# Performance work log

Hardware: AMD Instinct MI355X
Metric: run time of the kernel (lower is better)

## Reference

```python
import jax, jax.numpy as jnp
import numpy as np


def _ln(x):
    m = jnp.mean(x, axis=-1, keepdims=True)
    v = jnp.var(x, axis=-1, keepdims=True)
    return (x - m) * jax.lax.rsqrt(v + 1e-5)


def _forward(ql, cl, plm, ada_g_w, ada_g_b, ada_b_w, wq, bq, wk, wv, z_ln_g, z_ln_b, wz, wg, wo, sg_w, sg_b, ada2_g_w, ada2_g_b, ada2_b_w, ff1, ff2, ff3, sg2_w, sg2_b, n_queries, n_keys):
    B, N, C = ql.shape
    NB, _, D = wq.shape
    H = wz.shape[-1]
    DH = D // H
    # AF3-style 32x128 blocked local attention bias (additive mask), as in source
    centers = jnp.arange(N // n_queries + 1, dtype=jnp.float32) * n_queries + (n_queries / 2 - 0.5)
    pos = jnp.arange(N, dtype=jnp.float32)
    row = jnp.abs(pos[:, None] - centers[None, :]) < n_queries / 2   # [N, n_centers]
    col = jnp.abs(pos[:, None] - centers[None, :]) < n_keys / 2     # [N, n_centers]
    BIG = jnp.float32(1e10)
    blm = jnp.sum((row[:, None, :] & col[None, :, :]).astype(jnp.float32), axis=-1) * BIG - BIG  # [N, N], 0 or -1e10
    s_ln = _ln(cl)  # conditioning signal, shared LN across blocks
    a = ql
    for i in range(NB):  # DiffusionTransformer (AF3 Alg 23)
        # AttentionPairBias with AdaLN conditioning (Alg 24/26)
        x = jax.nn.sigmoid(s_ln @ ada_g_w[i] + ada_g_b[i]) * _ln(a) + s_ln @ ada_b_w[i]
        q = (x @ wq[i] + bq[i]).reshape(B, N, H, DH)
        k = (x @ wk[i]).reshape(B, N, H, DH)
        v = (x @ wv[i]).reshape(B, N, H, DH)
        zb = jnp.einsum('bqkc,ch->bhqk', _ln(plm) * z_ln_g[i] + z_ln_b[i], wz[i])  # pair bias
        logits = jnp.einsum('bqhd,bkhd->bhqk', q, k) * (1.0 / np.sqrt(DH)) + zb + blm[None, None]
        p = jax.nn.softmax(logits, axis=-1)
        o = jnp.einsum('bhqk,bkhd->bqhd', p, v)
        g = jax.nn.sigmoid(x @ wg[i]).reshape(B, N, H, DH)
        attn = (g * o).reshape(B, N, D) @ wo[i]
        b_out = jax.nn.sigmoid(s_ln @ sg_w[i] + sg_b[i]) * attn  # adaLN-zero style output gate
        # ConditionedTransitionBlock (Alg 25, SwiGLU)
        y = jax.nn.sigmoid(s_ln @ ada2_g_w[i] + ada2_g_b[i]) * _ln(a) + s_ln @ ada2_b_w[i]
        ff = jax.nn.silu(y @ ff1[i]) * (y @ ff2[i])
        t = jax.nn.sigmoid(s_ln @ sg2_w[i] + sg2_b[i]) * (ff @ ff3[i])
        a = b_out + t
    return a


def setup_inputs() -> dict:
    key = jax.random.key(0)
    B, N, C, CZ = 1, 3072, 128, 16
    H, DH, NB, CT = 4, 32, 3, 256  # CT = n_transition * C
    D = H * DH
    ks = jax.random.split(key, 32)
    it = iter(range(32))
    def r(shape, s=0.02):
        return jax.random.normal(ks[next(it)], shape, dtype=jnp.float32) * s
    inp = {
        'ql': jax.random.normal(ks[next(it)], (B, N, C), jnp.float32),
        'cl': jax.random.normal(ks[next(it)], (B, N, C), jnp.float32),
        'plm': jax.random.normal(ks[next(it)], (B, N, N, CZ), jnp.float32),
        'ada_g_w': r((NB, C, C)), 'ada_g_b': jnp.zeros((NB, C), jnp.float32), 'ada_b_w': r((NB, C, C)),
        'wq': r((NB, C, D)), 'bq': jnp.zeros((NB, D), jnp.float32), 'wk': r((NB, C, D)), 'wv': r((NB, C, D)),
        'z_ln_g': jnp.ones((NB, CZ), jnp.float32), 'z_ln_b': jnp.zeros((NB, CZ), jnp.float32), 'wz': r((NB, CZ, H)),
        'wg': r((NB, C, D)), 'wo': r((NB, D, C)),
        'sg_w': r((NB, C, C)), 'sg_b': jnp.full((NB, C), -2.0, jnp.float32),
        'ada2_g_w': r((NB, C, C)), 'ada2_g_b': jnp.zeros((NB, C), jnp.float32), 'ada2_b_w': r((NB, C, C)),
        'ff1': r((NB, C, CT)), 'ff2': r((NB, C, CT)), 'ff3': r((NB, CT, C)),
        'sg2_w': r((NB, C, C)), 'sg2_b': jnp.full((NB, C), -2.0, jnp.float32),
        'n_queries': 32, 'n_keys': 128,
    }
    return inp


def reference(ql, cl, plm, ada_g_w, ada_g_b, ada_b_w, wq, bq, wk, wv, z_ln_g, z_ln_b, wz, wg, wo, sg_w, sg_b, ada2_g_w, ada2_g_b, ada2_b_w, ff1, ff2, ff3, sg2_w, sg2_b, n_queries, n_keys):
    return _forward(ql, cl, plm, ada_g_w, ada_g_b, ada_b_w, wq, bq, wk, wv, z_ln_g, z_ln_b, wz, wg, wo, sg_w, sg_b, ada2_g_w, ada2_g_b, ada2_b_w, ff1, ff2, ff3, sg2_w, sg2_b, n_queries, n_keys)
```

## Files before the change

### kernel.cpp

```cpp
#include <hip/hip_runtime.h>
#include <cmath>

#define NTOK 3072
#define NBLK 3
#define PSS 133

__device__ __forceinline__ float sig(float v) { return 1.0f / (1.0f + expf(-v)); }

struct Params {
    const float *ql, *cl, *plm;
    const float *ada_g_w, *ada_g_b, *ada_b_w;
    const float *wq, *bq, *wk, *wv;
    const float *z_ln_g, *z_ln_b, *wz;
    const float *wg, *wo, *sg_w, *sg_b;
    const float *ada2_g_w, *ada2_g_b, *ada2_b_w;
    const float *ff1, *ff2, *ff3, *sg2_w, *sg2_b;
    float *anew, *attn, *qkvg, *ffb, *zb, *G;
    float *out;
};

__device__ __forceinline__ float4 ln_row32(float4 v)
{
    float s = v.x + v.y + v.z + v.w;
#pragma unroll
    for (int m = 1; m < 32; m <<= 1) s += __shfl_xor(s, m);
    float mean = s * (1.0f / 128.0f);
    float d0 = v.x - mean, d1 = v.y - mean, d2 = v.z - mean, d3 = v.w - mean;
    float var = d0 * d0 + d1 * d1 + d2 * d2 + d3 * d3;
#pragma unroll
    for (int m = 1; m < 32; m <<= 1) var += __shfl_xor(var, m);
    float rs = 1.0f / sqrtf(var * (1.0f / 128.0f) + 1e-5f);
    return make_float4(d0 * rs, d1 * rs, d2 * rs, d3 * rs);
}

__global__ __launch_bounds__(256) void k0_cond(Params P)
{
    int tid = threadIdx.x, bid = blockIdx.x;
    const size_t NC = (size_t)NTOK * 128;
    if (bid < 1728) {
        __shared__ __align__(16) float smA[32 * 132];
        int x8 = bid & 7, rest = bid >> 3;
        int tl = rest % 12, unit = rest / 12;
        int kind = unit % 6, i = unit / 6;
        int row0 = (x8 * 12 + tl) * 32;
#pragma unroll
        for (int it = 0; it < 4; it++) {
            int fo = (tid + it * 256) * 4, r = fo >> 7, c = fo & 127;
            *(float4*)&smA[r * 132 + c] = *(const float4*)&P.cl[(size_t)(row0 + r) * 128 + c];
        }
        __syncthreads();
        int hw = tid >> 5, cq = (tid & 31) * 4;
#pragma unroll
        for (int rr = 0; rr < 4; rr++) {
            int r = hw * 4 + rr;
            float4 n = ln_row32(*(float4*)&smA[r * 132 + cq]);
            *(float4*)&smA[r * 132 + cq] = n;
        }
        __syncthreads();
        const float* W; const float* bias = nullptr; bool dosig = false;
        switch (kind) {
            case 0:  W = P.ada_g_w  + (size_t)i * 16384; bias = P.ada_g_b  + i * 128; dosig = true; break;
            case 1:  W = P.ada_b_w  + (size_t)i * 16384; break;
            case 2:  W = P.ada2_g_w + (size_t)i * 16384; bias = P.ada2_g_b + i * 128; dosig = true; break;
            case 3:  W = P.ada2_b_w + (size_t)i * 16384; break;
            case 4:  W = P.sg_w     + (size_t)i * 16384; bias = P.sg_b     + i * 128; dosig = true; break;
            default: W = P.sg2_w    + (size_t)i * 16384; bias = P.sg2_b    + i * 128; dosig = true; break;
        }
        W += cq;
        float acc[4][4] = {};
#pragma unroll 8
        for (int k = 0; k < 128; k++) {
            float4 w4 = *(const float4*)(W + (size_t)k * 128);
#pragma unroll
            for (int rr = 0; rr < 4; rr++) {
                float a = smA[(hw * 4 + rr) * 132 + k];
                acc[rr][0] = fmaf(a, w4.x, acc[rr][0]);
                acc[rr][1] = fmaf(a, w4.y, acc[rr][1]);
                acc[rr][2] = fmaf(a, w4.z, acc[rr][2]);
                acc[rr][3] = fmaf(a, w4.w, acc[rr][3]);
            }
        }
        float4 b4 = bias ? *(const float4*)&bias[cq] : make_float4(0, 0, 0, 0);
        float* dst = P.G + (size_t)(kind * NBLK + i) * NC;
#pragma unroll
        for (int rr = 0; rr < 4; rr++) {
            float4 o = make_float4(acc[rr][0] + b4.x, acc[rr][1] + b4.y,
                                   acc[rr][2] + b4.z, acc[rr][3] + b4.w);
            if (dosig) { o.x = sig(o.x); o.y = sig(o.y); o.z = sig(o.z); o.w = sig(o.w); }
            *(float4*)&dst[(size_t)(row0 + hw * 4 + rr) * 128 + cq] = o;
        }
    } else {
        __shared__ __align__(16) float wzg[204];
        int b2 = bid - 1728;
        int x8 = b2 & 7, rest = b2 >> 3;
        int jl = rest >> 2, kkc = rest & 3;
        int j = x8 * 12 + jl;
        if (tid < 192) {
            int i3 = tid >> 6, rem = tid & 63, c = rem >> 2, h = rem & 3;
            wzg[(i3 * 16 + c) * 4 + h] = P.z_ln_g[i3 * 16 + c] * P.wz[(i3 * 16 + c) * 4 + h];
        }
        if (tid < 12) {
            int i3 = tid >> 2, h = tid & 3;
            float s = 0.0f;
            for (int c = 0; c < 16; c++) s += P.z_ln_b[i3 * 16 + c] * P.wz[(i3 * 16 + c) * 4 + h];
            wzg[192 + tid] = s;
        }
        __syncthreads();
        int kstart = max(0, j * 32 - 48);
        int W = min(NTOK, j * 32 + 80) - kstart;
#pragma unroll
        for (int it = 0; it < 4; it++) {
            int idx = tid + it * 256;
            int qi = idx >> 5, kk = kkc * 32 + (idx & 31);
            if (kk >= W) continue;
            int q = j * 32 + qi;
            const float* src = P.plm + ((size_t)q * NTOK + (size_t)(kstart + kk)) * 16;
            float xv[16];
            *(float4*)(xv + 0)  = *(const float4*)(src + 0);
            *(float4*)(xv + 4)  = *(const float4*)(src + 4);
            *(float4*)(xv + 8)  = *(const float4*)(src + 8);
            *(float4*)(xv + 12) = *(const float4*)(src + 12);
            float s = 0.0f;
#pragma unroll
            for (int c = 0; c < 16; c++) s += xv[c];
            float mean = s * (1.0f / 16.0f);
            float var = 0.0f;
#pragma unroll
            for (int c = 0; c < 16; c++) { float d = xv[c] - mean; var += d * d; }
            float rs = 1.0f / sqrtf(var * (1.0f / 16.0f) + 1e-5f);
#pragma unroll
            for (int c = 0; c < 16; c++) xv[c] = (xv[c] - mean) * rs;
#pragma unroll
            for (int i3 = 0; i3 < NBLK; i3++) {
#pragma unroll
                for (int h = 0; h < 4; h++) {
                    float o = wzg[192 + i3 * 4 + h];
#pragma unroll
                    for (int c = 0; c < 16; c++) o = fmaf(xv[c], wzg[(i3 * 16 + c) * 4 + h], o);
                    P.zb[((size_t)(i3 * 4 + h) * NTOK + q) * 128 + kk] = o;
                }
            }
        }
    }
}

__global__ __launch_bounds__(256) void k1_pre(Params P, int i)
{
    __shared__ __align__(16) float smX[16 * 132];
    const size_t NC = (size_t)NTOK * 128;
    int tid = threadIdx.x, bid = blockIdx.x;
    int x8 = bid & 7, rest = bid >> 3;
    int tl = rest % 24, u = rest / 24;
    int row0 = (x8 * 24 + tl) * 16;
    int sg = tid >> 5, cq = (tid & 31) * 4;
    const float* aprev = (i == 0) ? P.ql : P.anew;
    const float* Gg = P.G + (size_t)(((u < 4 ? 0 : 2) * NBLK) + i) * NC;
    const float* Gb = P.G + (size_t)(((u < 4 ? 1 : 3) * NBLK) + i) * NC;
#pragma unroll
    for (int rr = 0; rr < 2; rr++) {
        int r = row0 + sg * 2 + rr;
        float4 a4 = *(const float4*)&aprev[(size_t)r * 128 + cq];
        float4 ln4 = ln_row32(a4);
        float4 g4 = *(const float4*)&Gg[(size_t)r * 128 + cq];
        float4 b4 = *(const float4*)&Gb[(size_t)r * 128 + cq];
        float4 x4;
        x4.x = fmaf(g4.x, ln4.x, b4.x);
        x4.y = fmaf(g4.y, ln4.y, b4.y);
        x4.z = fmaf(g4.z, ln4.z, b4.z);
        x4.w = fmaf(g4.w, ln4.w, b4.w);
        *(float4*)&smX[(sg * 2 + rr) * 132 + cq] = x4;
    }
    __syncthreads();
    if (u < 4) {
        const float* W = (u == 0 ? P.wq : u == 1 ? P.wk : u == 2 ? P.wv : P.wg)
                         + (size_t)i * 16384 + cq;
        float acc[2][4] = {};
#pragma unroll 8
        for (int k = 0; k < 128; k++) {
            float4 w4 = *(const float4*)(W + (size_t)k * 128);
#pragma unroll
            for (int rr = 0; rr < 2; rr++) {
                float a = smX[(sg * 2 + rr) * 132 + k];
                acc[rr][0] = fmaf(a, w4.x, acc[rr][0]);
                acc[rr][1] = fmaf(a, w4.y, acc[rr][1]);
                acc[rr][2] = fmaf(a, w4.z, acc[rr][2]);
                acc[rr][3] = fmaf(a, w4.w, acc[rr][3]);
            }
        }
        float4 b4 = (u == 0) ? *(const float4*)&P.bq[(size_t)i * 128 + cq]
                             : make_float4(0, 0, 0, 0);
#pragma unroll
        for (int rr = 0; rr < 2; rr++) {
            int r = row0 + sg * 2 + rr;
            *(float4*)&P.qkvg[(size_t)r * 512 + u * 128 + cq] =
                make_float4(acc[rr][0] + b4.x, acc[rr][1] + b4.y,
                            acc[rr][2] + b4.z, acc[rr][3] + b4.w);
        }
    } else {
        int ch = (u - 4) * 128;
        const float* W1 = P.ff1 + (size_t)i * 32768 + ch + cq;
        const float* W2 = P.ff2 + (size_t)i * 32768 + ch + cq;
        float a1[2][4] = {}, a2[2][4] = {};
#pragma unroll 8
        for (int k = 0; k < 128; k++) {
            float4 w14 = *(const float4*)(W1 + (size_t)k * 256);
            float4 w24 = *(const float4*)(W2 + (size_t)k * 256);
#pragma unroll
            for (int rr = 0; rr < 2; rr++) {
                float a = smX[(sg * 2 + rr) * 132 + k];
                a1[rr][0] = fmaf(a, w14.x, a1[rr][0]);
                a1[rr][1] = fmaf(a, w14.y, a1[rr][1]);
                a1[rr][2] = fmaf(a, w14.z, a1[rr][2]);
                a1[rr][3] = fmaf(a, w14.w, a1[rr][3]);
                a2[rr][0] = fmaf(a, w24.x, a2[rr][0]);
                a2[rr][1] = fmaf(a, w24.y, a2[rr][1]);
                a2[rr][2] = fmaf(a, w24.z, a2[rr][2]);
                a2[rr][3] = fmaf(a, w24.w, a2[rr][3]);
            }
        }
#pragma unroll
        for (int rr = 0; rr < 2; rr++) {
            int r = row0 + sg * 2 + rr;
            float4 o;
            o.x = a1[rr][0] * sig(a1[rr][0]) * a2[rr][0];
            o.y = a1[rr][1] * sig(a1[rr][1]) * a2[rr][1];
            o.z = a1[rr][2] * sig(a1[rr][2]) * a2[rr][2];
            o.w = a1[rr][3] * sig(a1[rr][3]) * a2[rr][3];
            *(float4*)&P.ffb[(size_t)r * 256 + ch + cq] = o;
        }
    }
}

__global__ __launch_bounds__(256) void k2_attn(Params P, int i)
{
    __shared__ __align__(16) float ks[128 * 36];
    __shared__ __align__(16) float vs[128 * 36];
    __shared__ float ps[16 * PSS];
    int tid = threadIdx.x, bid = blockIdx.x;
    int x8 = bid & 7, g = bid >> 3;
    int jl = g >> 3, rem = g & 7;
    int h = rem >> 1, qh = rem & 1;
    int jglob = x8 * 12 + jl;
    int q0 = jglob * 32 + qh * 16;
    int kstart = max(0, jglob * 32 - 48);
    int W = min(NTOK, jglob * 32 + 80) - kstart;
    for (int idx = tid; idx < W * 8; idx += 256) {
        int kk = idx >> 3, d = (idx & 7) * 4;
        const float* base = &P.qkvg[(size_t)(kstart + kk) * 512 + 128 + h * 32 + d];
        float4 tK = *(const float4*)base;
        float4 tV = *(const float4*)(base + 128);
        *(float4*)&ks[kk * 36 + d] = tK;
        *(float4*)&vs[kk * 36 + d] = tV;
    }
    const float* zbase = &P.zb[((size_t)(i * 4 + h) * NTOK + q0) * 128];
#pragma unroll
    for (int it = 0; it < 2; it++) {
        int idx = tid + it * 256;
        int r = idx >> 5, c4 = (idx & 31) * 4;
        float4 z4 = *(const float4*)&zbase[(size_t)r * 128 + c4];
        ps[r * PSS + c4]     = z4.x;
        ps[r * PSS + c4 + 1] = z4.y;
        ps[r * PSS + c4 + 2] = z4.z;
        ps[r * PSS + c4 + 3] = z4.w;
    }
    int qi = tid & 15, kg = tid >> 4;
    float qreg[32];
    {
        const float* qp = &P.qkvg[(size_t)(q0 + qi) * 512 + h * 32];
#pragma unroll
        for (int d4 = 0; d4 < 8; d4++) {
            float4 tq = *(const float4*)(qp + d4 * 4);
            qreg[d4 * 4] = tq.x; qreg[d4 * 4 + 1] = tq.y;
            qreg[d4 * 4 + 2] = tq.z; qreg[d4 * 4 + 3] = tq.w;
        }
    }
    __syncthreads();
    const float scale = 0.17677669529663687f;
#pragma unroll
    for (int t2 = 0; t2 < 8; t2++) {
        int kk = kg + t2 * 16;
        if (kk < W) {
            float acc = 0.0f;
#pragma unroll
            for (int d4 = 0; d4 < 8; d4++) {
                float4 kv = *(const float4*)&ks[kk * 36 + d4 * 4];
                acc = fmaf(qreg[d4 * 4 + 0], kv.x, acc);
                acc = fmaf(qreg[d4 * 4 + 1], kv.y, acc);
                acc = fmaf(qreg[d4 * 4 + 2], kv.z, acc);
                acc = fmaf(qreg[d4 * 4 + 3], kv.w, acc);
            }
            ps[qi * PSS + kk] = fmaf(acc, scale, ps[qi * PSS + kk]);
        }
    }
    __syncthreads();
    {
        int row = tid >> 4, sub = tid & 15;
        float m = -3.0e38f;
        for (int kk = sub; kk < W; kk += 16) m = fmaxf(m, ps[row * PSS + kk]);
#pragma unroll
        for (int s2 = 1; s2 < 16; s2 <<= 1) m = fmaxf(m, __shfl_xor(m, s2));
        float ssum = 0.0f;
        for (int kk = sub; kk < W; kk += 16) {
            float e = expf(ps[row * PSS + kk] - m);
            ps[row * PSS + kk] = e; ssum += e;
        }
#pragma unroll
        for (int s2 = 1; s2 < 16; s2 <<= 1) ssum += __shfl_xor(ssum, s2);
        float rinv = 1.0f / ssum;
        for (int kk = sub; kk < W; kk += 16) ps[row * PSS + kk] *= rinv;
    }
    __syncthreads();
    {
        int dg = tid >> 4, d0 = dg * 2;
        float o0 = 0.0f, o1 = 0.0f, o0b = 0.0f, o1b = 0.0f;
        for (int kk = 0; kk + 1 < W; kk += 2) {
            float p0 = ps[qi * PSS + kk], p1 = ps[qi * PSS + kk + 1];
            float2 va = *(const float2*)&vs[kk * 36 + d0];
            float2 vb = *(const float2*)&vs[(kk + 1) * 36 + d0];
            o0  = fmaf(p0, va.x, o0);  o1  = fmaf(p0, va.y, o1);
            o0b = fmaf(p1, vb.x, o0b); o1b = fmaf(p1, vb.y, o1b);
        }
        if (W & 1) {
            float p0 = ps[qi * PSS + W - 1];
            float2 va = *(const float2*)&vs[(W - 1) * 36 + d0];
            o0 = fmaf(p0, va.x, o0); o1 = fmaf(p0, va.y, o1);
        }
        o0 += o0b; o1 += o1b;
        float2 g2 = *(const float2*)&P.qkvg[(size_t)(q0 + qi) * 512 + 384 + h * 32 + d0];
        *(float2*)&P.attn[(size_t)(q0 + qi) * 128 + h * 32 + d0] =
            make_float2(o0 * sig(g2.x), o1 * sig(g2.y));
    }
}

__global__ __launch_bounds__(256) void k3_post(Params P, int i)
{
    __shared__ __align__(16) float smB[16 * 132];
    __shared__ __align__(16) float smC[16 * 260];
    const size_t NC = (size_t)NTOK * 128;
    int tid = threadIdx.x, bid = blockIdx.x;
    int x8 = bid & 7, rest = bid >> 3;
    int tl = rest >> 2, cc = rest & 3;
    int row0 = x8 * 384 + tl * 16;
    int cbase = cc * 32;
#pragma unroll
    for (int it = 0; it < 2; it++) {
        int fo = (tid + it * 256) * 4, r = fo >> 7, c = fo & 127;
        *(float4*)&smB[r * 132 + c] = *(const float4*)&P.attn[(size_t)(row0 + r) * 128 + c];
    }
#pragma unroll
    for (int it = 0; it < 4; it++) {
        int fo = (tid + it * 256) * 4, r = fo >> 8, c = fo & 255;
        *(float4*)&smC[r * 260 + c] = *(const float4*)&P.ffb[(size_t)(row0 + r) * 256 + c];
    }
    __syncthreads();
    int r = tid >> 4, cl2 = (tid & 15) * 2;
    int c = cbase + cl2;
    const float* wo_p = P.wo  + (size_t)i * 16384 + c;
    const float* f3_p = P.ff3 + (size_t)i * 32768 + c;
    float aO0 = 0, aO1 = 0, aT0 = 0, aT1 = 0;
#pragma unroll 8
    for (int k = 0; k < 128; k++) {
        float2 w2 = *(const float2*)(wo_p + (size_t)k * 128);
        float a = smB[r * 132 + k];
        aO0 = fmaf(a, w2.x, aO0);
        aO1 = fmaf(a, w2.y, aO1);
    }
#pragma unroll 8
    for (int k = 0; k < 256; k++) {
        float2 w2 = *(const float2*)(f3_p + (size_t)k * 128);
        float a = smC[r * 260 + k];
        aT0 = fmaf(a, w2.x, aT0);
        aT1 = fmaf(a, w2.y, aT1);
    }
    int row = row0 + r;
    float2 sgv  = *(const float2*)&P.G[(size_t)(4 * NBLK + i) * NC + (size_t)row * 128 + c];
    float2 sg2v = *(const float2*)&P.G[(size_t)(5 * NBLK + i) * NC + (size_t)row * 128 + c];
    float2 o;
    o.x = sgv.x * aO0 + sg2v.x * aT0;
    o.y = sgv.y * aO1 + sg2v.y * aT1;
    float* dst = (i == NBLK - 1) ? P.out : P.anew;
    *(float2*)&dst[(size_t)row * 128 + c] = o;
}

extern "C" void kernel_launch(void* const* d_in, const int* in_sizes, int n_in,
                              void* d_out, int out_size, void* d_ws, size_t ws_size,
                              hipStream_t stream)
{
    Params P;
    P.ql       = (const float*)d_in[0];
    P.cl       = (const float*)d_in[1];
    P.plm      = (const float*)d_in[2];
    P.ada_g_w  = (const float*)d_in[3];
    P.ada_g_b  = (const float*)d_in[4];
    P.ada_b_w  = (const float*)d_in[5];
    P.wq       = (const float*)d_in[6];
    P.bq       = (const float*)d_in[7];
    P.wk       = (const float*)d_in[8];
    P.wv       = (const float*)d_in[9];
    P.z_ln_g   = (const float*)d_in[10];
    P.z_ln_b   = (const float*)d_in[11];
    P.wz       = (const float*)d_in[12];
    P.wg       = (const float*)d_in[13];
    P.wo       = (const float*)d_in[14];
    P.sg_w     = (const float*)d_in[15];
    P.sg_b     = (const float*)d_in[16];
    P.ada2_g_w = (const float*)d_in[17];
    P.ada2_g_b = (const float*)d_in[18];
    P.ada2_b_w = (const float*)d_in[19];
    P.ff1      = (const float*)d_in[20];
    P.ff2      = (const float*)d_in[21];
    P.ff3      = (const float*)d_in[22];
    P.sg2_w    = (const float*)d_in[23];
    P.sg2_b    = (const float*)d_in[24];

    float* ws = (float*)d_ws;
    const size_t NC = (size_t)NTOK * 128;
    P.anew = ws;
    P.attn = ws + NC;
    P.qkvg = ws + 2 * NC;
    P.ffb  = ws + 6 * NC;
    P.zb   = ws + 8 * NC;
    P.G    = ws + 20 * NC;
    P.out  = (float*)d_out;

    k0_cond<<<2112, 256, 0, stream>>>(P);
    for (int i = 0; i < NBLK; i++) {
        k1_pre<<<1152, 256, 0, stream>>>(P, i);
        k2_attn<<<768, 256, 0, stream>>>(P, i);
        k3_post<<<768, 256, 0, stream>>>(P, i);
    }
}
```

Baseline: 325.1 us.

## Fuse output projection into attention and defer residual sum to next pre-kernel

The wo projection is folded into the attention kernel, with each head writing a partial output to a per-head buffer. The ff3 projection now runs in extra blocks of the same launch, and the gated sum that forms the new activation is deferred into the next block's pre-kernel, plus a small final combine kernel. This drops one launch per block and the attn round trip through memory. The pre-kernel also processes 32 rows per block instead of 16 to reuse weights more. In exchange there is extra traffic for four head-partial buffers and more register pressure in the pre-kernel.

```diff
diff --git a/kernel.cpp b/kernel.cpp
--- a/kernel.cpp
+++ b/kernel.cpp
@@ -15,7 +15,7 @@
     const float *wg, *wo, *sg_w, *sg_b;
     const float *ada2_g_w, *ada2_g_b, *ada2_b_w;
     const float *ff1, *ff2, *ff3, *sg2_w, *sg2_b;
-    float *anew, *attn, *qkvg, *ffb, *zb, *G;
+    float *qkvg, *ffb, *zb, *G, *bout4, *tpart;
     float *out;
 };
 
@@ -144,22 +144,37 @@
     }
 }
 
-__global__ __launch_bounds__(256) void k1_pre(Params P, int i)
-{
-    __shared__ __align__(16) float smX[16 * 132];
+__global__ __launch_bounds__(256) void kA_pre(Params P, int i)
+{
+    __shared__ __align__(16) float smX[32 * 132];
     const size_t NC = (size_t)NTOK * 128;
     int tid = threadIdx.x, bid = blockIdx.x;
     int x8 = bid & 7, rest = bid >> 3;
-    int tl = rest % 24, u = rest / 24;
-    int row0 = (x8 * 24 + tl) * 16;
-    int sg = tid >> 5, cq = (tid & 31) * 4;
-    const float* aprev = (i == 0) ? P.ql : P.anew;
+    int tl = rest % 12, u = rest / 12;
+    int row0 = (x8 * 12 + tl) * 32;
+    int hw = tid >> 5, cq = (tid & 31) * 4;
     const float* Gg = P.G + (size_t)(((u < 4 ? 0 : 2) * NBLK) + i) * NC;
     const float* Gb = P.G + (size_t)(((u < 4 ? 1 : 3) * NBLK) + i) * NC;
-#pragma unroll
-    for (int rr = 0; rr < 2; rr++) {
-        int r = row0 + sg * 2 + rr;
-        float4 a4 = *(const float4*)&aprev[(size_t)r * 128 + cq];
+    const float* G4p = P.G + (size_t)(4 * NBLK + (i - 1)) * NC;
+#pragma unroll
+    for (int rr = 0; rr < 4; rr++) {
+        int r = row0 + hw * 4 + rr;
+        float4 a4;
+        if (i == 0) {
+            a4 = *(const float4*)&P.ql[(size_t)r * 128 + cq];
+        } else {
+            size_t off = (size_t)r * 128 + cq;
+            float4 p0 = *(const float4*)&P.bout4[off];
+            float4 p1 = *(const float4*)&P.bout4[NC + off];
+            float4 p2 = *(const float4*)&P.bout4[2 * NC + off];
+            float4 p3 = *(const float4*)&P.bout4[3 * NC + off];
+            float4 tp = *(const float4*)&P.tpart[off];
+            float4 gs = *(const float4*)&G4p[off];
+            a4.x = fmaf(gs.x, p0.x + p1.x + p2.x + p3.x, tp.x);
+            a4.y = fmaf(gs.y, p0.y + p1.y + p2.y + p3.y, tp.y);
+            a4.z = fmaf(gs.z, p0.z + p1.z + p2.z + p3.z, tp.z);
+            a4.w = fmaf(gs.w, p0.w + p1.w + p2.w + p3.w, tp.w);
+        }
         float4 ln4 = ln_row32(a4);
         float4 g4 = *(const float4*)&Gg[(size_t)r * 128 + cq];
         float4 b4 = *(const float4*)&Gb[(size_t)r * 128 + cq];
@@ -168,19 +183,19 @@
         x4.y = fmaf(g4.y, ln4.y, b4.y);
         x4.z = fmaf(g4.z, ln4.z, b4.z);
         x4.w = fmaf(g4.w, ln4.w, b4.w);
-        *(float4*)&smX[(sg * 2 + rr) * 132 + cq] = x4;
+        *(float4*)&smX[(hw * 4 + rr) * 132 + cq] = x4;
     }
     __syncthreads();
     if (u < 4) {
         const float* W = (u == 0 ? P.wq : u == 1 ? P.wk : u == 2 ? P.wv : P.wg)
                          + (size_t)i * 16384 + cq;
-        float acc[2][4] = {};
+        float acc[4][4] = {};
 #pragma unroll 8
         for (int k = 0; k < 128; k++) {
             float4 w4 = *(const float4*)(W + (size_t)k * 128);
 #pragma unroll
-            for (int rr = 0; rr < 2; rr++) {
-                float a = smX[(sg * 2 + rr) * 132 + k];
+            for (int rr = 0; rr < 4; rr++) {
+                float a = smX[(hw * 4 + rr) * 132 + k];
                 acc[rr][0] = fmaf(a, w4.x, acc[rr][0]);
                 acc[rr][1] = fmaf(a, w4.y, acc[rr][1]);
                 acc[rr][2] = fmaf(a, w4.z, acc[rr][2]);
@@ -190,8 +205,8 @@
         float4 b4 = (u == 0) ? *(const float4*)&P.bq[(size_t)i * 128 + cq]
                              : make_float4(0, 0, 0, 0);
 #pragma unroll
-        for (int rr = 0; rr < 2; rr++) {
-            int r = row0 + sg * 2 + rr;
+        for (int rr = 0; rr < 4; rr++) {
+            int r = row0 + hw * 4 + rr;
             *(float4*)&P.qkvg[(size_t)r * 512 + u * 128 + cq] =
                 make_float4(acc[rr][0] + b4.x, acc[rr][1] + b4.y,
                             acc[rr][2] + b4.z, acc[rr][3] + b4.w);
@@ -200,14 +215,14 @@
         int ch = (u - 4) * 128;
         const float* W1 = P.ff1 + (size_t)i * 32768 + ch + cq;
         const float* W2 = P.ff2 + (size_t)i * 32768 + ch + cq;
-        float a1[2][4] = {}, a2[2][4] = {};
-#pragma unroll 8
+        float a1[4][4] = {}, a2[4][4] = {};
+#pragma unroll 4
         for (int k = 0; k < 128; k++) {
             float4 w14 = *(const float4*)(W1 + (size_t)k * 256);
             float4 w24 = *(const float4*)(W2 + (size_t)k * 256);
 #pragma unroll
-            for (int rr = 0; rr < 2; rr++) {
-                float a = smX[(sg * 2 + rr) * 132 + k];
+            for (int rr = 0; rr < 4; rr++) {
+                float a = smX[(hw * 4 + rr) * 132 + k];
                 a1[rr][0] = fmaf(a, w14.x, a1[rr][0]);
                 a1[rr][1] = fmaf(a, w14.y, a1[rr][1]);
                 a1[rr][2] = fmaf(a, w14.z, a1[rr][2]);
@@ -219,8 +234,8 @@
             }
         }
 #pragma unroll
-        for (int rr = 0; rr < 2; rr++) {
-            int r = row0 + sg * 2 + rr;
+        for (int rr = 0; rr < 4; rr++) {
+            int r = row0 + hw * 4 + rr;
             float4 o;
             o.x = a1[rr][0] * sig(a1[rr][0]) * a2[rr][0];
             o.y = a1[rr][1] * sig(a1[rr][1]) * a2[rr][1];
@@ -231,155 +246,178 @@
     }
 }
 
-__global__ __launch_bounds__(256) void k2_attn(Params P, int i)
-{
-    __shared__ __align__(16) float ks[128 * 36];
-    __shared__ __align__(16) float vs[128 * 36];
-    __shared__ float ps[16 * PSS];
-    int tid = threadIdx.x, bid = blockIdx.x;
-    int x8 = bid & 7, g = bid >> 3;
-    int jl = g >> 3, rem = g & 7;
-    int h = rem >> 1, qh = rem & 1;
-    int jglob = x8 * 12 + jl;
-    int q0 = jglob * 32 + qh * 16;
-    int kstart = max(0, jglob * 32 - 48);
-    int W = min(NTOK, jglob * 32 + 80) - kstart;
-    for (int idx = tid; idx < W * 8; idx += 256) {
-        int kk = idx >> 3, d = (idx & 7) * 4;
-        const float* base = &P.qkvg[(size_t)(kstart + kk) * 512 + 128 + h * 32 + d];
-        float4 tK = *(const float4*)base;
-        float4 tV = *(const float4*)(base + 128);
-        *(float4*)&ks[kk * 36 + d] = tK;
-        *(float4*)&vs[kk * 36 + d] = tV;
-    }
-    const float* zbase = &P.zb[((size_t)(i * 4 + h) * NTOK + q0) * 128];
-#pragma unroll
-    for (int it = 0; it < 2; it++) {
-        int idx = tid + it * 256;
-        int r = idx >> 5, c4 = (idx & 31) * 4;
-        float4 z4 = *(const float4*)&zbase[(size_t)r * 128 + c4];
-        ps[r * PSS + c4]     = z4.x;
-        ps[r * PSS + c4 + 1] = z4.y;
-        ps[r * PSS + c4 + 2] = z4.z;
-        ps[r * PSS + c4 + 3] = z4.w;
-    }
-    int qi = tid & 15, kg = tid >> 4;
-    float qreg[32];
-    {
-        const float* qp = &P.qkvg[(size_t)(q0 + qi) * 512 + h * 32];
-#pragma unroll
-        for (int d4 = 0; d4 < 8; d4++) {
-            float4 tq = *(const float4*)(qp + d4 * 4);
-            qreg[d4 * 4] = tq.x; qreg[d4 * 4 + 1] = tq.y;
-            qreg[d4 * 4 + 2] = tq.z; qreg[d4 * 4 + 3] = tq.w;
-        }
-    }
-    __syncthreads();
-    const float scale = 0.17677669529663687f;
-#pragma unroll
-    for (int t2 = 0; t2 < 8; t2++) {
-        int kk = kg + t2 * 16;
-        if (kk < W) {
-            float acc = 0.0f;
-#pragma unroll
-            for (int d4 = 0; d4 < 8; d4++) {
-                float4 kv = *(const float4*)&ks[kk * 36 + d4 * 4];
-                acc = fmaf(qreg[d4 * 4 + 0], kv.x, acc);
-                acc = fmaf(qreg[d4 * 4 + 1], kv.y, acc);
-                acc = fmaf(qreg[d4 * 4 + 2], kv.z, acc);
-                acc = fmaf(qreg[d4 * 4 + 3], kv.w, acc);
-            }
-            ps[qi * PSS + kk] = fmaf(acc, scale, ps[qi * PSS + kk]);
-        }
-    }
-    __syncthreads();
-    {
-        int row = tid >> 4, sub = tid & 15;
-        float m = -3.0e38f;
-        for (int kk = sub; kk < W; kk += 16) m = fmaxf(m, ps[row * PSS + kk]);
-#pragma unroll
-        for (int s2 = 1; s2 < 16; s2 <<= 1) m = fmaxf(m, __shfl_xor(m, s2));
-        float ssum = 0.0f;
-        for (int kk = sub; kk < W; kk += 16) {
-            float e = expf(ps[row * PSS + kk] - m);
-            ps[row * PSS + kk] = e; ssum += e;
-        }
-#pragma unroll
-        for (int s2 = 1; s2 < 16; s2 <<= 1) ssum += __shfl_xor(ssum, s2);
-        float rinv = 1.0f / ssum;
-        for (int kk = sub; kk < W; kk += 16) ps[row * PSS + kk] *= rinv;
-    }
-    __syncthreads();
-    {
-        int dg = tid >> 4, d0 = dg * 2;
-        float o0 = 0.0f, o1 = 0.0f, o0b = 0.0f, o1b = 0.0f;
-        for (int kk = 0; kk + 1 < W; kk += 2) {
-            float p0 = ps[qi * PSS + kk], p1 = ps[qi * PSS + kk + 1];
-            float2 va = *(const float2*)&vs[kk * 36 + d0];
-            float2 vb = *(const float2*)&vs[(kk + 1) * 36 + d0];
-            o0  = fmaf(p0, va.x, o0);  o1  = fmaf(p0, va.y, o1);
-            o0b = fmaf(p1, vb.x, o0b); o1b = fmaf(p1, vb.y, o1b);
-        }
-        if (W & 1) {
-            float p0 = ps[qi * PSS + W - 1];
-            float2 va = *(const float2*)&vs[(W - 1) * 36 + d0];
-            o0 = fmaf(p0, va.x, o0); o1 = fmaf(p0, va.y, o1);
-        }
-        o0 += o0b; o1 += o1b;
-        float2 g2 = *(const float2*)&P.qkvg[(size_t)(q0 + qi) * 512 + 384 + h * 32 + d0];
-        *(float2*)&P.attn[(size_t)(q0 + qi) * 128 + h * 32 + d0] =
-            make_float2(o0 * sig(g2.x), o1 * sig(g2.y));
-    }
-}
-
-__global__ __launch_bounds__(256) void k3_post(Params P, int i)
-{
-    __shared__ __align__(16) float smB[16 * 132];
-    __shared__ __align__(16) float smC[16 * 260];
+__global__ __launch_bounds__(256) void kB_attn(Params P, int i)
+{
+    __shared__ __align__(16) float sm[11344];
     const size_t NC = (size_t)NTOK * 128;
     int tid = threadIdx.x, bid = blockIdx.x;
-    int x8 = bid & 7, rest = bid >> 3;
-    int tl = rest >> 2, cc = rest & 3;
-    int row0 = x8 * 384 + tl * 16;
-    int cbase = cc * 32;
-#pragma unroll
-    for (int it = 0; it < 2; it++) {
-        int fo = (tid + it * 256) * 4, r = fo >> 7, c = fo & 127;
-        *(float4*)&smB[r * 132 + c] = *(const float4*)&P.attn[(size_t)(row0 + r) * 128 + c];
+    if (bid < 768) {
+        float* ks = sm;
+        float* vs = sm + 4608;
+        float* ps = sm + 9216;
+        int x8 = bid & 7, g = bid >> 3;
+        int jl = g >> 3, rem = g & 7;
+        int h = rem >> 1, qh = rem & 1;
+        int jglob = x8 * 12 + jl;
+        int q0 = jglob * 32 + qh * 16;
+        int kstart = max(0, jglob * 32 - 48);
+        int W = min(NTOK, jglob * 32 + 80) - kstart;
+        for (int idx = tid; idx < W * 8; idx += 256) {
+            int kk = idx >> 3, d = (idx & 7) * 4;
+            const float* base = &P.qkvg[(size_t)(kstart + kk) * 512 + 128 + h * 32 + d];
+            float4 tK = *(const float4*)base;
+            float4 tV = *(const float4*)(base + 128);
+            *(float4*)&ks[kk * 36 + d] = tK;
+            *(float4*)&vs[kk * 36 + d] = tV;
+        }
+        const float* zbase = &P.zb[((size_t)(i * 4 + h) * NTOK + q0) * 128];
+#pragma unroll
+        for (int it = 0; it < 2; it++) {
+            int idx = tid + it * 256;
+            int r = idx >> 5, c4 = (idx & 31) * 4;
+            float4 z4 = *(const float4*)&zbase[(size_t)r * 128 + c4];
+            ps[r * PSS + c4]     = z4.x;
+            ps[r * PSS + c4 + 1] = z4.y;
+            ps[r * PSS + c4 + 2] = z4.z;
+            ps[r * PSS + c4 + 3] = z4.w;
+        }
+        int qi = tid & 15, kg = tid >> 4;
+        float qreg[32];
+        {
+            const float* qp = &P.qkvg[(size_t)(q0 + qi) * 512 + h * 32];
+#pragma unroll
+            for (int d4 = 0; d4 < 8; d4++) {
+                float4 tq = *(const float4*)(qp + d4 * 4);
+                qreg[d4 * 4] = tq.x; qreg[d4 * 4 + 1] = tq.y;
+                qreg[d4 * 4 + 2] = tq.z; qreg[d4 * 4 + 3] = tq.w;
+            }
+        }
+        __syncthreads();
+        const float scale = 0.17677669529663687f;
+#pragma unroll
+        for (int t2 = 0; t2 < 8; t2++) {
+            int kk = kg + t2 * 16;
+            if (kk < W) {
+                float acc = 0.0f;
+#pragma unroll
+                for (int d4 = 0; d4 < 8; d4++) {
+                    float4 kv = *(const float4*)&ks[kk * 36 + d4 * 4];
+                    acc = fmaf(qreg[d4 * 4 + 0], kv.x, acc);
+                    acc = fmaf(qreg[d4 * 4 + 1], kv.y, acc);
+                    acc = fmaf(qreg[d4 * 4 + 2], kv.z, acc);
+                    acc = fmaf(qreg[d4 * 4 + 3], kv.w, acc);
+                }
+                ps[qi * PSS + kk] = fmaf(acc, scale, ps[qi * PSS + kk]);
+            }
+        }
+        __syncthreads();
+        {
+            int row = tid >> 4, sub = tid & 15;
+            float m = -3.0e38f;
+            for (int kk = sub; kk < W; kk += 16) m = fmaxf(m, ps[row * PSS + kk]);
+#pragma unroll
+            for (int s2 = 1; s2 < 16; s2 <<= 1) m = fmaxf(m, __shfl_xor(m, s2));
+            float ssum = 0.0f;
+            for (int kk = sub; kk < W; kk += 16) {
+                float e = expf(ps[row * PSS + kk] - m);
+                ps[row * PSS + kk] = e; ssum += e;
+            }
+#pragma unroll
+            for (int s2 = 1; s2 < 16; s2 <<= 1) ssum += __shfl_xor(ssum, s2);
+            float rinv = 1.0f / ssum;
+            for (int kk = sub; kk < W; kk += 16) ps[row * PSS + kk] *= rinv;
+        }
+        __syncthreads();
+        {
+            int dg = tid >> 4, d0 = dg * 2;
+            float o0 = 0.0f, o1 = 0.0f, o0b = 0.0f, o1b = 0.0f;
+            for (int kk = 0; kk + 1 < W; kk += 2) {
+                float p0 = ps[qi * PSS + kk], p1 = ps[qi * PSS + kk + 1];
+                float2 va = *(const float2*)&vs[kk * 36 + d0];
+                float2 vb = *(const float2*)&vs[(kk + 1) * 36 + d0];
+                o0  = fmaf(p0, va.x, o0);  o1  = fmaf(p0, va.y, o1);
+                o0b = fmaf(p1, vb.x, o0b); o1b = fmaf(p1, vb.y, o1b);
+            }
+            if (W & 1) {
+                float p0 = ps[qi * PSS + W - 1];
+                float2 va = *(const float2*)&vs[(W - 1) * 36 + d0];
+                o0 = fmaf(p0, va.x, o0); o1 = fmaf(p0, va.y, o1);
+            }
+            o0 += o0b; o1 += o1b;
+            float2 g2 = *(const float2*)&P.qkvg[(size_t)(q0 + qi) * 512 + 384 + h * 32 + d0];
+            ks[qi * 33 + d0]     = o0 * sig(g2.x);
+            ks[qi * 33 + d0 + 1] = o1 * sig(g2.y);
+        }
+        __syncthreads();
+        {
+            int r = tid >> 4, ci = tid & 15;
+            int c0 = ci * 8;
+            const float* o_s = ks;
+            const float* wop = P.wo + (size_t)i * 16384 + (size_t)(h * 32) * 128 + c0;
+            float acc[8] = {};
+#pragma unroll 4
+            for (int d = 0; d < 32; d++) {
+                float a = o_s[r * 33 + d];
+                float4 w0 = *(const float4*)(wop + (size_t)d * 128);
+                float4 w1 = *(const float4*)(wop + (size_t)d * 128 + 4);
+                acc[0] = fmaf(a, w0.x, acc[0]); acc[1] = fmaf(a, w0.y, acc[1]);
+                acc[2] = fmaf(a, w0.z, acc[2]); acc[3] = fmaf(a, w0.w, acc[3]);
+                acc[4] = fmaf(a, w1.x, acc[4]); acc[5] = fmaf(a, w1.y, acc[5]);
+                acc[6] = fmaf(a, w1.z, acc[6]); acc[7] = fmaf(a, w1.w, acc[7]);
+            }
+            float* dst = P.bout4 + (size_t)h * NC + (size_t)(q0 + r) * 128 + c0;
+            *(float4*)dst       = make_float4(acc[0], acc[1], acc[2], acc[3]);
+            *(float4*)(dst + 4) = make_float4(acc[4], acc[5], acc[6], acc[7]);
+        }
+    } else {
+        float* smC = sm;
+        int b2 = bid - 768;
+        int x8 = b2 & 7, rest = b2 >> 3;
+        int tl = rest >> 1, chalf = rest & 1;
+        int row0 = x8 * 384 + tl * 16;
+#pragma unroll
+        for (int it = 0; it < 4; it++) {
+            int fo = (tid + it * 256) * 4, r = fo >> 8, c = fo & 255;
+            *(float4*)&smC[r * 260 + c] = *(const float4*)&P.ffb[(size_t)(row0 + r) * 256 + c];
+        }
+        __syncthreads();
+        int r = tid >> 4, c = chalf * 64 + (tid & 15) * 4;
+        const float* f3_p = P.ff3 + (size_t)i * 32768 + c;
+        float acc[4] = {};
+#pragma unroll 8
+        for (int k = 0; k < 256; k++) {
+            float4 w4 = *(const float4*)(f3_p + (size_t)k * 128);
+            float a = smC[r * 260 + k];
+            acc[0] = fmaf(a, w4.x, acc[0]);
+            acc[1] = fmaf(a, w4.y, acc[1]);
+            acc[2] = fmaf(a, w4.z, acc[2]);
+            acc[3] = fmaf(a, w4.w, acc[3]);
+        }
+        int row = row0 + r;
+        float4 g5 = *(const float4*)&P.G[(size_t)(5 * NBLK + i) * NC + (size_t)row * 128 + c];
+        *(float4*)&P.tpart[(size_t)row * 128 + c] =
+            make_float4(g5.x * acc[0], g5.y * acc[1], g5.z * acc[2], g5.w * acc[3]);
     }
-#pragma unroll
-    for (int it = 0; it < 4; it++) {
-        int fo = (tid + it * 256) * 4, r = fo >> 8, c = fo & 255;
-        *(float4*)&smC[r * 260 + c] = *(const float4*)&P.ffb[(size_t)(row0 + r) * 256 + c];
-    }
-    __syncthreads();
-    int r = tid >> 4, cl2 = (tid & 15) * 2;
-    int c = cbase + cl2;
-    const float* wo_p = P.wo  + (size_t)i * 16384 + c;
-    const float* f3_p = P.ff3 + (size_t)i * 32768 + c;
-    float aO0 = 0, aO1 = 0, aT0 = 0, aT1 = 0;
-#pragma unroll 8
-    for (int k = 0; k < 128; k++) {
-        float2 w2 = *(const float2*)(wo_p + (size_t)k * 128);
-        float a = smB[r * 132 + k];
-        aO0 = fmaf(a, w2.x, aO0);
-        aO1 = fmaf(a, w2.y, aO1);
-    }
-#pragma unroll 8
-    for (int k = 0; k < 256; k++) {
-        float2 w2 = *(const float2*)(f3_p + (size_t)k * 128);
-        float a = smC[r * 260 + k];
-        aT0 = fmaf(a, w2.x, aT0);
-        aT1 = fmaf(a, w2.y, aT1);
-    }
-    int row = row0 + r;
-    float2 sgv  = *(const float2*)&P.G[(size_t)(4 * NBLK + i) * NC + (size_t)row * 128 + c];
-    float2 sg2v = *(const float2*)&P.G[(size_t)(5 * NBLK + i) * NC + (size_t)row * 128 + c];
-    float2 o;
-    o.x = sgv.x * aO0 + sg2v.x * aT0;
-    o.y = sgv.y * aO1 + sg2v.y * aT1;
-    float* dst = (i == NBLK - 1) ? P.out : P.anew;
-    *(float2*)&dst[(size_t)row * 128 + c] = o;
+}
+
+__global__ __launch_bounds__(256) void kC_out(Params P)
+{
+    const size_t NC = (size_t)NTOK * 128;
+    int idx = blockIdx.x * 256 + threadIdx.x;
+    int r = idx >> 5, cq = (idx & 31) * 4;
+    size_t off = (size_t)r * 128 + cq;
+    float4 p0 = *(const float4*)&P.bout4[off];
+    float4 p1 = *(const float4*)&P.bout4[NC + off];
+    float4 p2 = *(const float4*)&P.bout4[2 * NC + off];
+    float4 p3 = *(const float4*)&P.bout4[3 * NC + off];
+    float4 tp = *(const float4*)&P.tpart[off];
+    float4 gs = *(const float4*)&P.G[(size_t)(4 * NBLK + (NBLK - 1)) * NC + off];
+    float4 o;
+    o.x = fmaf(gs.x, p0.x + p1.x + p2.x + p3.x, tp.x);
+    o.y = fmaf(gs.y, p0.y + p1.y + p2.y + p3.y, tp.y);
+    o.z = fmaf(gs.z, p0.z + p1.z + p2.z + p3.z, tp.z);
+    o.w = fmaf(gs.w, p0.w + p1.w + p2.w + p3.w, tp.w);
+    *(float4*)&P.out[off] = o;
 }
 
 extern "C" void kernel_launch(void* const* d_in, const int* in_sizes, int n_in,
@@ -415,18 +453,18 @@
 
     float* ws = (float*)d_ws;
     const size_t NC = (size_t)NTOK * 128;
-    P.anew = ws;
-    P.attn = ws + NC;
-    P.qkvg = ws + 2 * NC;
-    P.ffb  = ws + 6 * NC;
-    P.zb   = ws + 8 * NC;
-    P.G    = ws + 20 * NC;
-    P.out  = (float*)d_out;
+    P.qkvg  = ws;
+    P.ffb   = ws + 4 * NC;
+    P.zb    = ws + 6 * NC;
+    P.G     = ws + 18 * NC;
+    P.bout4 = ws + 36 * NC;
+    P.tpart = ws + 40 * NC;
+    P.out   = (float*)d_out;
 
     k0_cond<<<2112, 256, 0, stream>>>(P);
     for (int i = 0; i < NBLK; i++) {
-        k1_pre<<<1152, 256, 0, stream>>>(P, i);
-        k2_attn<<<768, 256, 0, stream>>>(P, i);
-        k3_post<<<768, 256, 0, stream>>>(P, i);
+        kA_pre<<<576, 256, 0, stream>>>(P, i);
+        kB_attn<<<1152, 256, 0, stream>>>(P, i);
     }
-}
+    kC_out<<<384, 256, 0, stream>>>(P);
+}
```

Measured after the change: 264.1 us. 1.23x faster.
